# Kernel tuning notes

Hardware: AMD Instinct MI355X
Metric: run time of the kernel (lower is better)

Reference implementation:

```python
import jax, jax.numpy as jnp
import numpy as np

B, N, D_IN, D_HID, N_ITER = 32, 512, 256, 128, 10


def setup_inputs() -> dict:
    key = jax.random.key(0)
    ks = jax.random.split(key, 8)
    s = 1.0 / np.sqrt(D_IN)  # torch Linear default init range
    return {
        "Xh": jax.random.normal(ks[0], (B, N, D_IN), jnp.float32),
        "Xm": jax.random.normal(ks[1], (B, N, D_IN), jnp.float32),
        # position 0 is the root; tokens 1..len are valid
        "lengths": jax.random.randint(ks[2], (B,), N // 2, N),
        "Wh": jax.random.uniform(ks[3], (D_HID, D_IN), jnp.float32, -s, s),
        "bh": jax.random.uniform(ks[4], (D_HID,), jnp.float32, -s, s),
        "Wm": jax.random.uniform(ks[5], (D_HID, D_IN), jnp.float32, -s, s),
        "bm": jax.random.uniform(ks[6], (D_HID,), jnp.float32, -s, s),
        "V": 0.01 * jax.random.normal(ks[7], (D_HID, D_HID), jnp.float32),
    }


def _logZ(scores, lengths):
    """Matrix-tree log-partition for single-root nonprojective trees.

    scores: [B,N,N] arc scores, scores[b,h,m] = head h -> modifier m, index 0 = root.
    lengths: [B] number of real tokens (valid modifiers at 1..len).
    """
    Bn, Nn, _ = scores.shape
    idx = jnp.arange(Nn)
    tok = (idx[None, :] >= 1) & (idx[None, :] <= lengths[:, None])   # [B,N] valid modifiers
    head = idx[None, :] <= lengths[:, None]                          # [B,N] valid heads (incl. root)
    pair = head[:, :, None] & tok[:, None, :] & (idx[:, None] != idx[None, :])
    # stability shift: every tree has exactly `len` edges, so logZ shifts by len*c
    c = jax.lax.stop_gradient(
        jnp.max(jnp.where(pair, scores, -jnp.inf), axis=(1, 2)))
    A = jnp.where(pair, jnp.exp(scores - c[:, None, None]), 0.0)     # [B,N,N]
    r = A[:, 0, 1:]                                                  # root -> token weights [B,N-1]
    At = A[:, 1:, 1:]                                                # token -> token weights
    ar = jnp.arange(Nn - 1)
    # Laplacian L = diag(colsum) - At (diag of At is zero by pair mask)
    Lap = (-At).at[:, ar, ar].set(r + At.sum(axis=1))
    # Koo et al. (2007): replace first row with root weights
    Lhat = Lap.at[:, 0, :].set(r)
    # padded positions: identity rows to keep det unchanged
    Lhat = Lhat.at[:, ar, ar].add(jnp.where(tok[:, 1:], 0.0, 1.0))
    _, logabs = jnp.linalg.slogdet(Lhat)
    return logabs + lengths.astype(scores.dtype) * c


def _marginals(scores, lengths):
    """nonprojective_marginals: (logZ, entropy, mu) via grad of logZ."""
    def f(s):
        lz = _logZ(s, lengths)
        return lz.sum(), lz
    (_, logZ), Y = jax.value_and_grad(f, has_aux=True)(scores)
    entr = logZ - jnp.sum(Y * scores, axis=(1, 2))
    return logZ, entr, Y


def reference(Xh, Xm, lengths, Wh, bh, Wm, bm, V):
    # dropout=0 -> H_mask/M_mask are ones
    H0 = Xh @ Wh.T + bh          # h_mlp(Xh), invariant across iterations
    M0 = Xm @ Wm.T + bm          # m_mlp(Xm)
    H = jax.nn.relu(H0)
    M = jax.nn.relu(M0)
    scores = jnp.einsum("bhu,uv,bmv->bhm", H, V, M)
    logZ, entr, Y = _marginals(scores, lengths)
    for _ in range(1, N_ITER):
        Hn = jax.nn.relu(H0 + Y @ M @ V.T)                       # _update_H
        Mn = jax.nn.relu(M0 + jnp.swapaxes(Y, -2, -1) @ H @ V)   # _update_M
        scores = jnp.einsum("bhu,uv,bmv->bhm", Hn, V, Mn)
        logZ, entr, Y = _marginals(scores, lengths)
        H, M = Hn, Mn
    return scores, logZ, Y, entr
```

## Files before the change

kernel.cpp:

```cpp
#include <hip/hip_runtime.h>
#include <math.h>

constexpr int BB = 32;
constexpr int NN_ = 512;
constexpr int DIN = 256;
constexpr int DH = 128;
constexpr int NITER = 10;
constexpr long HSTR = (long)NN_ * DH;
constexpr long SSTR = (long)NN_ * NN_;
constexpr long LSTR = 512L * 512L;

__device__ __forceinline__ unsigned f2mono(float f) {
    unsigned u = __float_as_uint(f);
    return (u & 0x80000000u) ? ~u : (u | 0x80000000u);
}
__device__ __forceinline__ float mono2f(unsigned u) {
    return __uint_as_float((u & 0x80000000u) ? (u & 0x7fffffffu) : ~u);
}

__device__ __forceinline__ float invert128(float r[8][8], int tid,
        float (*RowP)[8][132], float (*ColPT)[8][132], float (*Rnew)[8][132])
{
    int tx = tid & 15, ty = tid >> 4;
    int lane = tid & 63, w = tid >> 6;
    int li = lane >> 3, lj = lane & 7;
    float lacc = 0.f;
    __syncthreads();
    for (int s8 = 0; s8 < 16; ++s8) {
        int p = s8 & 1;
        if (ty == s8) {
            #pragma unroll
            for (int i = 0; i < 8; ++i)
                #pragma unroll
                for (int j = 0; j < 8; ++j)
                    RowP[p][i][tx * 8 + j] = r[i][j];
        }
        if (tx == s8) {
            float sub = (ty == s8) ? 1.f : 0.f;
            #pragma unroll
            for (int i = 0; i < 8; ++i)
                #pragma unroll
                for (int j = 0; j < 8; ++j)
                    ColPT[p][j][ty * 8 + i] = r[i][j] - ((i == j) ? sub : 0.f);
        }
        __syncthreads();
        float d = RowP[p][li][s8 * 8 + lj];
        float prod = 1.f;
        #pragma unroll
        for (int s = 0; s < 8; ++s) {
            float pv = __shfl(d, s * 9);
            prod *= pv;
            float pinv = 1.0f / pv;
            float rv = __shfl(d, s * 8 + lj);
            float cv = __shfl(d, li * 8 + s);
            float nd;
            if (li == s && lj == s)  nd = pinv;
            else if (li == s)        nd = rv * pinv;
            else if (lj == s)        nd = -cv * pinv;
            else                     nd = d - cv * pinv * rv;
            d = nd;
        }
        lacc += logf(fabsf(prod));
        {
            int sr = li;
            int jq = w * 32 + lj * 4;
            float dsr[8];
            #pragma unroll
            for (int t = 0; t < 8; ++t) dsr[t] = __shfl(d, (lane & 56) + t);
            float a0 = 0.f, a1 = 0.f, a2 = 0.f, a3 = 0.f;
            #pragma unroll
            for (int t = 0; t < 8; ++t) {
                float4 rp = *(const float4*)&RowP[p][t][jq];
                a0 += dsr[t] * rp.x; a1 += dsr[t] * rp.y;
                a2 += dsr[t] * rp.z; a3 += dsr[t] * rp.w;
            }
            if ((jq >> 3) == s8) {
                if ((jq & 7) == 0) {
                    a0 = dsr[0] + ((sr == 0) ? 1.f : 0.f);
                    a1 = dsr[1] + ((sr == 1) ? 1.f : 0.f);
                    a2 = dsr[2] + ((sr == 2) ? 1.f : 0.f);
                    a3 = dsr[3] + ((sr == 3) ? 1.f : 0.f);
                } else {
                    a0 = dsr[4] + ((sr == 4) ? 1.f : 0.f);
                    a1 = dsr[5] + ((sr == 5) ? 1.f : 0.f);
                    a2 = dsr[6] + ((sr == 6) ? 1.f : 0.f);
                    a3 = dsr[7] + ((sr == 7) ? 1.f : 0.f);
                }
            }
            *(float4*)&Rnew[p][sr][jq] = make_float4(a0, a1, a2, a3);
        }
        __syncthreads();
        #pragma unroll
        for (int t = 0; t < 8; ++t) {
            float cp[8], rn[8];
            *(float4*)&cp[0] = *(const float4*)&ColPT[p][t][ty * 8];
            *(float4*)&cp[4] = *(const float4*)&ColPT[p][t][ty * 8 + 4];
            *(float4*)&rn[0] = *(const float4*)&Rnew[p][t][tx * 8];
            *(float4*)&rn[4] = *(const float4*)&Rnew[p][t][tx * 8 + 4];
            #pragma unroll
            for (int i = 0; i < 8; ++i)
                #pragma unroll
                for (int j = 0; j < 8; ++j)
                    r[i][j] -= cp[i] * rn[j];
        }
    }
    return lacc;
}

template<int AMODE, int BMODE, int EPI>
__global__ __launch_bounds__(256) void gemm64(
    const float* __restrict__ A, const float* __restrict__ Bm,
    float* __restrict__ C, const float* __restrict__ Dp, float* __restrict__ C2,
    int Mdim, int Ndim, int Kdim,
    long sA, long sB, long sC, long sD)
{
    constexpr int BK = 16;
    __shared__ float As[BK][64 + 4];
    __shared__ float Bs[BK][64 + 4];
    int b = blockIdx.z;
    const float* Ab = A + (long)b * sA;
    const float* Bb = Bm + (long)b * sB;
    int m0 = blockIdx.x * 64, n0 = blockIdx.y * 64;
    int tid = threadIdx.x;
    int tx = tid & 15, ty = tid >> 4;
    float acc[4][4] = {};

    int arow, acol, brow, bcol;
    if (AMODE == 0) { arow = tid >> 2; acol = (tid & 3) * 4; }
    else            { arow = tid >> 4; acol = (tid & 15) * 4; }
    if (BMODE == 0) { brow = tid >> 4; bcol = (tid & 15) * 4; }
    else            { brow = tid >> 2; bcol = (tid & 3) * 4; }

    float4 av, bv;
    if (AMODE == 0) av = *(const float4*)(Ab + (long)(m0 + arow) * Kdim + acol);
    else            av = *(const float4*)(Ab + (long)(0 + arow) * Mdim + m0 + acol);
    if (BMODE == 0) bv = *(const float4*)(Bb + (long)(0 + brow) * Ndim + n0 + bcol);
    else            bv = *(const float4*)(Bb + (long)(n0 + brow) * Kdim + bcol);

    for (int k0 = 0; k0 < Kdim; k0 += BK) {
        __syncthreads();
        if (AMODE == 0) {
            As[acol + 0][arow] = av.x; As[acol + 1][arow] = av.y;
            As[acol + 2][arow] = av.z; As[acol + 3][arow] = av.w;
        } else {
            *(float4*)&As[arow][acol] = av;
        }
        if (BMODE == 0) {
            *(float4*)&Bs[brow][bcol] = bv;
        } else {
            Bs[bcol + 0][brow] = bv.x; Bs[bcol + 1][brow] = bv.y;
            Bs[bcol + 2][brow] = bv.z; Bs[bcol + 3][brow] = bv.w;
        }
        float4 av2, bv2;
        if (k0 + BK < Kdim) {
            int k1 = k0 + BK;
            if (AMODE == 0) av2 = *(const float4*)(Ab + (long)(m0 + arow) * Kdim + k1 + acol);
            else            av2 = *(const float4*)(Ab + (long)(k1 + arow) * Mdim + m0 + acol);
            if (BMODE == 0) bv2 = *(const float4*)(Bb + (long)(k1 + brow) * Ndim + n0 + bcol);
            else            bv2 = *(const float4*)(Bb + (long)(n0 + brow) * Kdim + k1 + bcol);
        }
        __syncthreads();
        #pragma unroll
        for (int k = 0; k < BK; ++k) {
            float4 a4 = *(const float4*)&As[k][ty * 4];
            float4 b4 = *(const float4*)&Bs[k][tx * 4];
            float avv[4] = {a4.x, a4.y, a4.z, a4.w};
            float bvv[4] = {b4.x, b4.y, b4.z, b4.w};
            #pragma unroll
            for (int i = 0; i < 4; ++i)
                #pragma unroll
                for (int j = 0; j < 4; ++j)
                    acc[i][j] += avv[i] * bvv[j];
        }
        av = av2; bv = bv2;
    }

    int r0 = m0 + ty * 4, c0 = n0 + tx * 4;
    if (EPI == 0) {
        float* Cb = C + (long)b * sC;
        #pragma unroll
        for (int i = 0; i < 4; ++i)
            *(float4*)(Cb + (long)(r0 + i) * Ndim + c0) =
                make_float4(acc[i][0], acc[i][1], acc[i][2], acc[i][3]);
    } else if (EPI == 1) {
        float4 bias = *(const float4*)(Dp + c0);
        float bb4[4] = {bias.x, bias.y, bias.z, bias.w};
        #pragma unroll
        for (int i = 0; i < 4; ++i) {
            float pre[4];
            #pragma unroll
            for (int j = 0; j < 4; ++j) pre[j] = acc[i][j] + bb4[j];
            *(float4*)(C2 + (long)(r0 + i) * Ndim + c0) =
                make_float4(pre[0], pre[1], pre[2], pre[3]);
            *(float4*)(C + (long)(r0 + i) * Ndim + c0) =
                make_float4(fmaxf(pre[0], 0.f), fmaxf(pre[1], 0.f),
                            fmaxf(pre[2], 0.f), fmaxf(pre[3], 0.f));
        }
    } else {
        const float* Db = Dp + (long)b * sD;
        float* Cb = C + (long)b * sC;
        #pragma unroll
        for (int i = 0; i < 4; ++i) {
            float4 d = *(const float4*)(Db + (long)(r0 + i) * Ndim + c0);
            float pre[4] = {acc[i][0] + d.x, acc[i][1] + d.y,
                            acc[i][2] + d.z, acc[i][3] + d.w};
            *(float4*)(Cb + (long)(r0 + i) * Ndim + c0) =
                make_float4(fmaxf(pre[0], 0.f), fmaxf(pre[1], 0.f),
                            fmaxf(pre[2], 0.f), fmaxf(pre[3], 0.f));
        }
    }
}

__global__ __launch_bounds__(256) void score_gemm(
    const float* __restrict__ A, const float* __restrict__ Bm,
    float* __restrict__ C, const int* __restrict__ len,
    unsigned* __restrict__ cu)
{
    int b = blockIdx.z;
    const float* Ab = A + (long)b * HSTR;
    const float* Bb = Bm + (long)b * HSTR;
    int m0 = blockIdx.x * 128, n0 = blockIdx.y * 128;
    int tid = threadIdx.x, tx = tid & 15, ty = tid >> 4;
    __shared__ float As[8][132];
    __shared__ float Bs[8][132];
    float acc[8][8] = {};
    int row = tid >> 1, kq = (tid & 1) << 2;
    float4 av = *(const float4*)(Ab + (long)(m0 + row) * DH + kq);
    float4 bv = *(const float4*)(Bb + (long)(n0 + row) * DH + kq);
    for (int kc = 0; kc < DH; kc += 8) {
        __syncthreads();
        As[kq + 0][row] = av.x; As[kq + 1][row] = av.y;
        As[kq + 2][row] = av.z; As[kq + 3][row] = av.w;
        Bs[kq + 0][row] = bv.x; Bs[kq + 1][row] = bv.y;
        Bs[kq + 2][row] = bv.z; Bs[kq + 3][row] = bv.w;
        float4 av2, bv2;
        if (kc + 8 < DH) {
            av2 = *(const float4*)(Ab + (long)(m0 + row) * DH + kc + 8 + kq);
            bv2 = *(const float4*)(Bb + (long)(n0 + row) * DH + kc + 8 + kq);
        }
        __syncthreads();
        #pragma unroll
        for (int k = 0; k < 8; ++k) {
            float a[8], bb[8];
            *(float4*)&a[0] = *(float4*)&As[k][ty * 8];
            *(float4*)&a[4] = *(float4*)&As[k][ty * 8 + 4];
            *(float4*)&bb[0] = *(float4*)&Bs[k][tx * 8];
            *(float4*)&bb[4] = *(float4*)&Bs[k][tx * 8 + 4];
            #pragma unroll
            for (int i = 0; i < 8; ++i)
                #pragma unroll
                for (int j = 0; j < 8; ++j) acc[i][j] += a[i] * bb[j];
        }
        av = av2; bv = bv2;
    }
    int L = len[b];
    float vmax = -3.0e38f;
    float* Cb = C + (long)b * SSTR;
    #pragma unroll
    for (int i = 0; i < 8; ++i) {
        int h = m0 + ty * 8 + i;
        bool hok = (h <= L);
        *(float4*)(Cb + (long)h * NN_ + n0 + tx * 8) =
            make_float4(acc[i][0], acc[i][1], acc[i][2], acc[i][3]);
        *(float4*)(Cb + (long)h * NN_ + n0 + tx * 8 + 4) =
            make_float4(acc[i][4], acc[i][5], acc[i][6], acc[i][7]);
        #pragma unroll
        for (int j = 0; j < 8; ++j) {
            int m = n0 + tx * 8 + j;
            if (hok && m >= 1 && m <= L && m != h) vmax = fmaxf(vmax, acc[i][j]);
        }
    }
    __syncthreads();
    float* red = &As[0][0];
    red[tid] = vmax; __syncthreads();
    for (int off = 128; off; off >>= 1) {
        if (tid < off) red[tid] = fmaxf(red[tid], red[tid + off]);
        __syncthreads();
    }
    if (tid == 0) atomicMax(&cu[b], f2mono(red[0]));
}

__global__ void zero_scal(float* scal) {
    if (threadIdx.x < 96) scal[threadIdx.x] = 0.f;
}

__global__ __launch_bounds__(256) void colsum_k(const float* __restrict__ sc,
                                                const int* __restrict__ len,
                                                const unsigned* __restrict__ cu,
                                                float* __restrict__ colsum)
{
    int b = blockIdx.x, yb = blockIdx.y;
    int tid = threadIdx.x, lane = tid & 63, w = tid >> 6;
    int L = len[b];
    float c = mono2f(cu[b]);
    int m = yb * 64 + lane;
    const float* S = sc + (long)b * SSTR;
    float s = 0.f;
    bool mv = (m >= 1 && m <= L);
    if (mv) {
        for (int h = 1 + w; h < NN_; h += 4) {
            if (h <= L && h != m) s += expf(S[(long)h * NN_ + m] - c);
        }
    }
    __shared__ float part[4][64];
    part[w][lane] = s; __syncthreads();
    if (tid < 64)
        colsum[(long)b * NN_ + yb * 64 + tid] =
            part[0][tid] + part[1][tid] + part[2][tid] + part[3][tid];
}

__global__ __launch_bounds__(256) void build_rows(const float* __restrict__ sc,
                                                  const int* __restrict__ len,
                                                  const unsigned* __restrict__ cu,
                                                  const float* __restrict__ colsum,
                                                  float* __restrict__ Lm,
                                                  float* __restrict__ Fb0,
                                                  float* __restrict__ logdet)
{
    __shared__ float sm[6][8][132];
    int b = blockIdx.x;
    int tid = threadIdx.x;
    int L = len[b];
    float c = mono2f(cu[b]);
    const float* S = sc + (long)b * SSTR;
    const float* cs = colsum + (long)b * NN_;

    if (blockIdx.y == 0) {
        int tx = tid & 15, ty = tid >> 4;
        float r[8][8];
        #pragma unroll
        for (int i = 0; i < 8; ++i) {
            int gi = ty * 8 + i;
            #pragma unroll
            for (int j = 0; j < 8; ++j) {
                int gj = tx * 8 + j;
                int tm = gj + 1;
                bool mv = (tm <= L);
                float v;
                if (gi == 0) {
                    v = mv ? expf(S[tm] - c) : 0.f;
                } else if (gi == gj) {
                    float rv = mv ? expf(S[tm] - c) : 0.f;
                    v = rv + cs[tm] + (mv ? 0.f : 1.f);
                } else {
                    int h = gi + 1;
                    v = (h <= L && mv) ? -expf(S[(long)h * NN_ + tm] - c) : 0.f;
                }
                r[i][j] = v;
            }
        }
        float lacc = invert128(r, tid,
                               (float(*)[8][132])&sm[0],
                               (float(*)[8][132])&sm[2],
                               (float(*)[8][132])&sm[4]);
        float* Ab = Lm + (long)b * LSTR;
        #pragma unroll
        for (int i = 0; i < 8; ++i) {
            *(float4*)(Ab + (long)(ty * 8 + i) * 512 + tx * 8) =
                make_float4(r[i][0], r[i][1], r[i][2], r[i][3]);
            *(float4*)(Ab + (long)(ty * 8 + i) * 512 + tx * 8 + 4) =
                make_float4(r[i][4], r[i][5], r[i][6], r[i][7]);
        }
        if (tid == 0) atomicAdd(&logdet[b], lacc);
        return;
    }

    int i0 = (blockIdx.y - 1) * 8;
    #pragma unroll
    for (int r = 0; r < 8; ++r) {
        int i = i0 + r;
        float* Lrow = Lm + (long)b * LSTR + (long)i * 512;
        float* Frow = Fb0 + (long)b * HSTR + (long)i * 128;
        #pragma unroll
        for (int q = 0; q < 2; ++q) {
            int j = tid + q * 256;
            float v;
            if (i == 511 || j == 511) {
                v = (i == j) ? 1.f : 0.f;
            } else {
                int tm = j + 1;
                bool mv = (tm <= L);
                if (i == 0) {
                    v = mv ? expf(S[tm] - c) : 0.f;
                } else if (i == j) {
                    float rv = mv ? expf(S[tm] - c) : 0.f;
                    v = rv + cs[tm] + ((tm > L) ? 1.f : 0.f);
                } else {
                    int h = i + 1;
                    v = (h <= L && mv) ? -expf(S[(long)h * NN_ + tm] - c) : 0.f;
                }
            }
            if (!(i < 128 && j < 128)) Lrow[j] = v;
            if (q == 0 && j < 128 && i >= 128) Frow[j] = v;
        }
    }
}

__global__ __launch_bounds__(256) void gj_panel(float* __restrict__ Lm,
                                                float* __restrict__ Fnext, int kb)
{
    int b = blockIdx.x, j = blockIdx.y;
    int jt = j + (j >= kb);
    int tid = threadIdx.x;
    float* base = Lm + (long)b * LSTR;
    const float* D = base + (long)(kb * 128) * 512 + kb * 128;
    float* Aj = base + (long)(kb * 128) * 512 + jt * 128;
    __shared__ float Ds_[8][132];
    __shared__ float Asj[8][132];
    int tx = tid & 15, ty = tid >> 4;
    int drow = tid >> 1, dkq = (tid & 1) << 2;
    int akr = tid >> 5, acq = (tid & 31) << 2;
    float acc[8][8] = {};
    float4 dv = *(const float4*)(D + (long)drow * 512 + dkq);
    float4 ajv = *(const float4*)(Aj + (long)akr * 512 + acq);
    for (int kc = 0; kc < 128; kc += 8) {
        __syncthreads();
        Ds_[dkq + 0][drow] = dv.x; Ds_[dkq + 1][drow] = dv.y;
        Ds_[dkq + 2][drow] = dv.z; Ds_[dkq + 3][drow] = dv.w;
        *(float4*)&Asj[akr][acq] = ajv;
        float4 dv2, ajv2;
        if (kc + 8 < 128) {
            dv2 = *(const float4*)(D + (long)drow * 512 + kc + 8 + dkq);
            ajv2 = *(const float4*)(Aj + (long)(kc + 8 + akr) * 512 + acq);
        }
        __syncthreads();
        #pragma unroll
        for (int k = 0; k < 8; ++k) {
            float a[8], bv[8];
            *(float4*)&a[0] = *(float4*)&Ds_[k][ty * 8];
            *(float4*)&a[4] = *(float4*)&Ds_[k][ty * 8 + 4];
            *(float4*)&bv[0] = *(float4*)&Asj[k][tx * 8];
            *(float4*)&bv[4] = *(float4*)&Asj[k][tx * 8 + 4];
            #pragma unroll
            for (int i = 0; i < 8; ++i)
                #pragma unroll
                for (int jj = 0; jj < 8; ++jj) acc[i][jj] += a[i] * bv[jj];
        }
        dv = dv2; ajv = ajv2;
    }
    bool dual = (jt == kb + 1);
    float* Fn = Fnext + (long)b * HSTR + (long)(kb * 128) * 128;
    #pragma unroll
    for (int i = 0; i < 8; ++i) {
        float4 o0 = make_float4(acc[i][0], acc[i][1], acc[i][2], acc[i][3]);
        float4 o1 = make_float4(acc[i][4], acc[i][5], acc[i][6], acc[i][7]);
        *(float4*)(Aj + (long)(ty * 8 + i) * 512 + tx * 8) = o0;
        *(float4*)(Aj + (long)(ty * 8 + i) * 512 + tx * 8 + 4) = o1;
        if (dual) {
            *(float4*)(Fn + (long)(ty * 8 + i) * 128 + tx * 8) = o0;
            *(float4*)(Fn + (long)(ty * 8 + i) * 128 + tx * 8 + 4) = o1;
        }
    }
}

template<int FUSE>
__global__ __launch_bounds__(256) void gj_update(float* __restrict__ Lm,
                                                 const float* __restrict__ Fbuf,
                                                 float* __restrict__ Fnext,
                                                 float* __restrict__ logdet, int kb)
{
    __shared__ float sm[FUSE ? 6 : 2][8][132];
    int b = blockIdx.x;
    int it = blockIdx.y;
    int jt = blockIdx.z;
    int ib = it + (it >= kb);
    int tid = threadIdx.x, tx = tid & 15, ty = tid >> 4;
    float* base = Lm + (long)b * LSTR;
    const float* F = Fbuf + (long)b * HSTR + (long)(ib * 128) * 128;
    const float* R = base + (long)(kb * 128) * 512 + jt * 128;
    float* Cb = base + (long)(ib * 128) * 512 + jt * 128;
    float (*Fs)[132] = sm[0];
    float (*Rs)[132] = sm[1];
    int frow = tid >> 1, fkq = (tid & 1) << 2;
    int rkr = tid >> 5, rcq = (tid & 31) << 2;
    float acc[8][8] = {};
    float4 fv = *(const float4*)(F + (long)frow * 128 + fkq);
    float4 rv = *(const float4*)(R + (long)rkr * 512 + rcq);
    for (int kc = 0; kc < 128; kc += 8) {
        __syncthreads();
        Fs[fkq + 0][frow] = fv.x; Fs[fkq + 1][frow] = fv.y;
        Fs[fkq + 2][frow] = fv.z; Fs[fkq + 3][frow] = fv.w;
        *(float4*)&Rs[rkr][rcq] = rv;
        float4 fv2, rv2;
        if (kc + 8 < 128) {
            fv2 = *(const float4*)(F + (long)frow * 128 + kc + 8 + fkq);
            rv2 = *(const float4*)(R + (long)(kc + 8 + rkr) * 512 + rcq);
        }
        __syncthreads();
        #pragma unroll
        for (int k = 0; k < 8; ++k) {
            float a[8], bv[8];
            *(float4*)&a[0] = *(float4*)&Fs[k][ty * 8];
            *(float4*)&a[4] = *(float4*)&Fs[k][ty * 8 + 4];
            *(float4*)&bv[0] = *(float4*)&Rs[k][tx * 8];
            *(float4*)&bv[4] = *(float4*)&Rs[k][tx * 8 + 4];
            #pragma unroll
            for (int i = 0; i < 8; ++i)
                #pragma unroll
                for (int j = 0; j < 8; ++j) acc[i][j] += a[i] * bv[j];
        }
        fv = fv2; rv = rv2;
    }
    if (FUSE && ib == kb + 1 && jt == kb + 1) {
        #pragma unroll
        for (int i = 0; i < 8; ++i) {
            float4 o0 = *(const float4*)(Cb + (long)(ty * 8 + i) * 512 + tx * 8);
            float4 o1 = *(const float4*)(Cb + (long)(ty * 8 + i) * 512 + tx * 8 + 4);
            acc[i][0] = o0.x - acc[i][0]; acc[i][1] = o0.y - acc[i][1];
            acc[i][2] = o0.z - acc[i][2]; acc[i][3] = o0.w - acc[i][3];
            acc[i][4] = o1.x - acc[i][4]; acc[i][5] = o1.y - acc[i][5];
            acc[i][6] = o1.z - acc[i][6]; acc[i][7] = o1.w - acc[i][7];
        }
        float lacc = invert128(acc, tid,
                               (float(*)[8][132])&sm[0],
                               (float(*)[8][132])&sm[FUSE ? 2 : 0],
                               (float(*)[8][132])&sm[FUSE ? 4 : 0]);
        #pragma unroll
        for (int i = 0; i < 8; ++i) {
            *(float4*)(Cb + (long)(ty * 8 + i) * 512 + tx * 8) =
                make_float4(acc[i][0], acc[i][1], acc[i][2], acc[i][3]);
            *(float4*)(Cb + (long)(ty * 8 + i) * 512 + tx * 8 + 4) =
                make_float4(acc[i][4], acc[i][5], acc[i][6], acc[i][7]);
        }
        if (tid == 0) atomicAdd(&logdet[b], lacc);
        return;
    }
    bool dual = (jt == kb + 1);
    float* Fn = Fnext + (long)b * HSTR + (long)(ib * 128) * 128;
    if (jt == kb) {
        #pragma unroll
        for (int i = 0; i < 8; ++i) {
            *(float4*)(Cb + (long)(ty * 8 + i) * 512 + tx * 8) =
                make_float4(-acc[i][0], -acc[i][1], -acc[i][2], -acc[i][3]);
            *(float4*)(Cb + (long)(ty * 8 + i) * 512 + tx * 8 + 4) =
                make_float4(-acc[i][4], -acc[i][5], -acc[i][6], -acc[i][7]);
        }
    } else {
        #pragma unroll
        for (int i = 0; i < 8; ++i) {
            float4 o0 = *(const float4*)(Cb + (long)(ty * 8 + i) * 512 + tx * 8);
            float4 o1 = *(const float4*)(Cb + (long)(ty * 8 + i) * 512 + tx * 8 + 4);
            o0 = make_float4(o0.x - acc[i][0], o0.y - acc[i][1],
                             o0.z - acc[i][2], o0.w - acc[i][3]);
            o1 = make_float4(o1.x - acc[i][4], o1.y - acc[i][5],
                             o1.z - acc[i][6], o1.w - acc[i][7]);
            *(float4*)(Cb + (long)(ty * 8 + i) * 512 + tx * 8) = o0;
            *(float4*)(Cb + (long)(ty * 8 + i) * 512 + tx * 8 + 4) = o1;
            if (dual) {
                *(float4*)(Fn + (long)(ty * 8 + i) * 128 + tx * 8) = o0;
                *(float4*)(Fn + (long)(ty * 8 + i) * 128 + tx * 8 + 4) = o1;
            }
        }
    }
}

__global__ __launch_bounds__(256) void y_k(const float* __restrict__ sc,
                                           const float* __restrict__ Binv,
                                           const int* __restrict__ len,
                                           const unsigned* __restrict__ cu,
                                           float* __restrict__ Y,
                                           float* __restrict__ Ssum)
{
    int b = blockIdx.x;
    int ht = blockIdx.y >> 3, mt = blockIdx.y & 7;
    int h0 = ht * 64, m0 = mt * 64;
    int tid = threadIdx.x;
    int L = len[b];
    float c = mono2f(cu[b]);
    const float* S = sc + (long)b * SSTR;
    const float* Bi = Binv + (long)b * LSTR;
    float* Yb = Y + (long)b * SSTR;
    __shared__ float Bs[64][65];
    __shared__ float Ds[64], C0s[64];
    {
        int hh = tid & 63, m4 = tid >> 6;
        int col = h0 + hh - 1;
        for (int mm = m4; mm < 64; mm += 4) {
            int row = m0 + mm - 1;
            Bs[mm][hh] = (row >= 0 && col >= 0) ? Bi[(long)row * 512 + col] : 0.f;
        }
    }
    if (tid < 64) {
        int row = m0 + tid - 1;
        Ds[tid] = (row >= 0) ? Bi[(long)row * 512 + row] : 0.f;
    } else if (tid < 128) {
        int mm = tid - 64, row = m0 + mm - 1;
        C0s[mm] = (row >= 0) ? Bi[(long)row * 512] : 0.f;
    }
    __syncthreads();
    int mm = tid & 63, hq = tid >> 6;
    int m = m0 + mm;
    float lsum = 0.f;
    bool mvalid = (m >= 1 && m <= L);
    float dterm = (m >= 2) ? Ds[mm] : 0.f;
    #pragma unroll
    for (int hi = 0; hi < 16; ++hi) {
        int hh = hq * 16 + hi;
        int h = h0 + hh;
        float s = S[(long)h * NN_ + m];
        float y = 0.f;
        if (mvalid && h <= L && h != m) {
            float a = expf(s - c);
            float g;
            if (h == 0) g = C0s[mm] + dterm;
            else g = dterm - ((h >= 2) ? Bs[mm][hh] : 0.f);
            y = a * g;
        }
        Yb[(long)h * NN_ + m] = y;
        lsum += y * s;
    }
    __shared__ float red[256];
    red[tid] = lsum; __syncthreads();
    for (int off = 128; off; off >>= 1) {
        if (tid < off) red[tid] += red[tid + off];
        __syncthreads();
    }
    if (tid == 0) atomicAdd(&Ssum[b], red[0]);
}

__global__ void fin_k(const int* __restrict__ len, unsigned* __restrict__ cu,
                      float* __restrict__ logdet, float* __restrict__ Ssum,
                      float* __restrict__ outLogZ, float* __restrict__ outEntr)
{
    int b = threadIdx.x;
    if (b < 32) {
        float c = mono2f(cu[b]);
        float lz = logdet[b] + (float)len[b] * c;
        outLogZ[b] = lz;
        outEntr[b] = lz - Ssum[b];
        cu[b] = 0u;
        logdet[b] = 0.f;
        Ssum[b] = 0.f;
    }
}

extern "C" void kernel_launch(void* const* d_in, const int* in_sizes, int n_in,
                              void* d_out, int out_size, void* d_ws, size_t ws_size,
                              hipStream_t stream)
{
    const float* Xh = (const float*)d_in[0];
    const float* Xm = (const float*)d_in[1];
    const int*   len = (const int*)d_in[2];
    const float* Wh = (const float*)d_in[3];
    const float* bh = (const float*)d_in[4];
    const float* Wm = (const float*)d_in[5];
    const float* bm = (const float*)d_in[6];
    const float* V  = (const float*)d_in[7];

    float* ws = (float*)d_ws;
    constexpr long U = 2097152;
    float* H0 = ws;
    float* M0 = ws + U;
    float* Ha = ws + 2 * U;
    float* Ma = ws + 3 * U;
    float* Hb = ws + 4 * U;
    float* Mb = ws + 5 * U;
    float* T1 = ws + 6 * U;
    float* Yt = ws + 7 * U;
    float* Lm = ws + 8 * U;
    float* cs = ws + 12 * U;
    float* scal = ws + 12 * U + 16384;
    unsigned* cu = (unsigned*)scal;
    float* logdet = scal + 32;
    float* Ssum = scal + 64;

    float* Sout = (float*)d_out;
    float* outLogZ = (float*)d_out + 8388608;
    float* Yout = (float*)d_out + 8388640;
    float* outEntr = (float*)d_out + 8388640 + 8388608;

    zero_scal<<<1, 96, 0, stream>>>(scal);

    gemm64<0,1,1><<<dim3(256, 2, 1), 256, 0, stream>>>(
        Xh, Wh, Ha, bh, H0, 16384, DH, DIN, 0, 0, 0, 0);
    gemm64<0,1,1><<<dim3(256, 2, 1), 256, 0, stream>>>(
        Xm, Wm, Ma, bm, M0, 16384, DH, DIN, 0, 0, 0, 0);

    float* Hc = Ha; float* Mc = Ma; float* Hn = Hb; float* Mn = Mb;
    for (int t = 0; t < NITER; ++t) {
        if (t > 0) {
            gemm64<0,1,0><<<dim3(8,2,BB),256,0,stream>>>(
                Mc, V, Yt, nullptr, nullptr, 512, DH, DH, HSTR, 0, HSTR, 0);
            gemm64<0,0,2><<<dim3(8,2,BB),256,0,stream>>>(
                Yout, Yt, Hn, H0, nullptr, 512, DH, 512, SSTR, HSTR, HSTR, HSTR);
            gemm64<1,0,2><<<dim3(8,2,BB),256,0,stream>>>(
                Yout, T1, Mn, M0, nullptr, 512, DH, 512, SSTR, HSTR, HSTR, HSTR);
            { float* tmp = Hc; Hc = Hn; Hn = tmp; }
            { float* tmp = Mc; Mc = Mn; Mn = tmp; }
        }
        gemm64<0,0,0><<<dim3(8,2,BB),256,0,stream>>>(
            Hc, V, T1, nullptr, nullptr, 512, DH, DH, HSTR, 0, HSTR, 0);
        score_gemm<<<dim3(4,4,BB),256,0,stream>>>(T1, Mc, Sout, len, cu);

        colsum_k<<<dim3(BB,8),256,0,stream>>>(Sout, len, cu, cs);
        build_rows<<<dim3(BB,65),256,0,stream>>>(Sout, len, cu, cs, Lm, Yt, logdet);

        float* Fbufs[2] = {Yt, Hn};
        for (int kb = 0; kb < 4; ++kb) {
            float* Fcur  = Fbufs[kb & 1];
            float* Fnext = Fbufs[(kb + 1) & 1];
            gj_panel<<<dim3(BB,3),256,0,stream>>>(Lm, Fnext, kb);
            if (kb < 3)
                gj_update<1><<<dim3(BB,3,4),256,0,stream>>>(Lm, Fcur, Fnext, logdet, kb);
            else
                gj_update<0><<<dim3(BB,3,4),256,0,stream>>>(Lm, Fcur, Fnext, logdet, kb);
        }
        y_k<<<dim3(BB,64),256,0,stream>>>(Sout, Lm, len, cu, Yout, Ssum);
        fin_k<<<1,32,0,stream>>>(len, cu, logdet, Ssum, outLogZ, outEntr);
    }
}
```

Measured before the change: 5.692 ms.

## Move diagonal block inversion into panel kernel and widen GJ kernels to 512 threads

The 128x128 diagonal-block inversion moves out of the tail of gj_update, where a single block ran it serially, and into the start of the panel kernel. Every panel block now redundantly inverts the pivot block held in registers, and only block 0 writes it back and adds to logdet. Both the panel and update GEMMs switch to 512 threads with 8x4 per-thread tiles and a K-step of 16, aiming for more parallelism and shorter serial tails. The cost is that the inversion is computed three times per batch, and invert128 runs with half the threads idle.

```diff
diff --git a/kernel.cpp b/kernel.cpp
--- a/kernel.cpp
+++ b/kernel.cpp
@@ -24,18 +24,19 @@
     int tx = tid & 15, ty = tid >> 4;
     int lane = tid & 63, w = tid >> 6;
     int li = lane >> 3, lj = lane & 7;
+    const bool act = (tid < 256);
     float lacc = 0.f;
     __syncthreads();
     for (int s8 = 0; s8 < 16; ++s8) {
         int p = s8 & 1;
-        if (ty == s8) {
+        if (act && ty == s8) {
             #pragma unroll
             for (int i = 0; i < 8; ++i)
                 #pragma unroll
                 for (int j = 0; j < 8; ++j)
                     RowP[p][i][tx * 8 + j] = r[i][j];
         }
-        if (tx == s8) {
+        if (act && tx == s8) {
             float sub = (ty == s8) ? 1.f : 0.f;
             #pragma unroll
             for (int i = 0; i < 8; ++i)
@@ -61,7 +62,7 @@
             d = nd;
         }
         lacc += logf(fabsf(prod));
-        {
+        if (act) {
             int sr = li;
             int jq = w * 32 + lj * 4;
             float dsr[8];
@@ -90,18 +91,20 @@
             *(float4*)&Rnew[p][sr][jq] = make_float4(a0, a1, a2, a3);
         }
         __syncthreads();
-        #pragma unroll
-        for (int t = 0; t < 8; ++t) {
-            float cp[8], rn[8];
-            *(float4*)&cp[0] = *(const float4*)&ColPT[p][t][ty * 8];
-            *(float4*)&cp[4] = *(const float4*)&ColPT[p][t][ty * 8 + 4];
-            *(float4*)&rn[0] = *(const float4*)&Rnew[p][t][tx * 8];
-            *(float4*)&rn[4] = *(const float4*)&Rnew[p][t][tx * 8 + 4];
-            #pragma unroll
-            for (int i = 0; i < 8; ++i)
-                #pragma unroll
-                for (int j = 0; j < 8; ++j)
-                    r[i][j] -= cp[i] * rn[j];
+        if (act) {
+            #pragma unroll
+            for (int t = 0; t < 8; ++t) {
+                float cp[8], rn[8];
+                *(float4*)&cp[0] = *(const float4*)&ColPT[p][t][ty * 8];
+                *(float4*)&cp[4] = *(const float4*)&ColPT[p][t][ty * 8 + 4];
+                *(float4*)&rn[0] = *(const float4*)&Rnew[p][t][tx * 8];
+                *(float4*)&rn[4] = *(const float4*)&Rnew[p][t][tx * 8 + 4];
+                #pragma unroll
+                for (int i = 0; i < 8; ++i)
+                    #pragma unroll
+                    for (int j = 0; j < 8; ++j)
+                        r[i][j] -= cp[i] * rn[j];
+            }
         }
     }
     return lacc;
@@ -396,160 +399,161 @@
     }
 }
 
-__global__ __launch_bounds__(256) void gj_panel(float* __restrict__ Lm,
-                                                float* __restrict__ Fnext, int kb)
-{
+__global__ __launch_bounds__(512) void gj_panel_inv(
+    float* __restrict__ Lm, const float* __restrict__ Fcur,
+    float* __restrict__ Fnext, float* __restrict__ logdet, int kb)
+{
+    __shared__ float sm[6 * 8 * 132];
+    float (*Ds)[132]  = (float (*)[132])sm;
+    float (*Asj)[132] = (float (*)[132])(sm + 16 * 132);
     int b = blockIdx.x, j = blockIdx.y;
     int jt = j + (j >= kb);
     int tid = threadIdx.x;
+    int tx = tid & 15, ty = tid >> 4;
     float* base = Lm + (long)b * LSTR;
-    const float* D = base + (long)(kb * 128) * 512 + kb * 128;
+    float r[8][8] = {};
+    if (kb == 0) {
+        if (tid < 256) {
+            const float* D0 = base;
+            #pragma unroll
+            for (int i = 0; i < 8; ++i) {
+                *(float4*)&r[i][0] = *(const float4*)(D0 + (long)(ty * 8 + i) * 512 + tx * 8);
+                *(float4*)&r[i][4] = *(const float4*)(D0 + (long)(ty * 8 + i) * 512 + tx * 8 + 4);
+            }
+        }
+    } else {
+        if (tid < 256) {
+            const float* T = Fcur + (long)b * HSTR + (long)(kb * 128) * 128;
+            #pragma unroll
+            for (int i = 0; i < 8; ++i) {
+                *(float4*)&r[i][0] = *(const float4*)(T + (long)(ty * 8 + i) * 128 + tx * 8);
+                *(float4*)&r[i][4] = *(const float4*)(T + (long)(ty * 8 + i) * 128 + tx * 8 + 4);
+            }
+        }
+        float lacc = invert128(r, tid,
+                               (float (*)[8][132])sm,
+                               (float (*)[8][132])(sm + 2 * 8 * 132),
+                               (float (*)[8][132])(sm + 4 * 8 * 132));
+        if (j == 0) {
+            if (tid < 256) {
+                float* Dd = base + (long)(kb * 128) * 512 + kb * 128;
+                #pragma unroll
+                for (int i = 0; i < 8; ++i) {
+                    *(float4*)(Dd + (long)(ty * 8 + i) * 512 + tx * 8) =
+                        make_float4(r[i][0], r[i][1], r[i][2], r[i][3]);
+                    *(float4*)(Dd + (long)(ty * 8 + i) * 512 + tx * 8 + 4) =
+                        make_float4(r[i][4], r[i][5], r[i][6], r[i][7]);
+                }
+            }
+            if (tid == 0) atomicAdd(&logdet[b], lacc);
+        }
+    }
+
+    int tx2 = tid & 31, ty2 = tid >> 5;
     float* Aj = base + (long)(kb * 128) * 512 + jt * 128;
-    __shared__ float Ds_[8][132];
-    __shared__ float Asj[8][132];
-    int tx = tid & 15, ty = tid >> 4;
-    int drow = tid >> 1, dkq = (tid & 1) << 2;
     int akr = tid >> 5, acq = (tid & 31) << 2;
-    float acc[8][8] = {};
-    float4 dv = *(const float4*)(D + (long)drow * 512 + dkq);
+    float acc[8][4] = {};
     float4 ajv = *(const float4*)(Aj + (long)akr * 512 + acq);
-    for (int kc = 0; kc < 128; kc += 8) {
-        __syncthreads();
-        Ds_[dkq + 0][drow] = dv.x; Ds_[dkq + 1][drow] = dv.y;
-        Ds_[dkq + 2][drow] = dv.z; Ds_[dkq + 3][drow] = dv.w;
+    for (int kc = 0; kc < 128; kc += 16) {
+        __syncthreads();
+        if (tid < 256 && (tx >> 1) == (kc >> 4)) {
+            int kloc = (tx & 1) * 8;
+            #pragma unroll
+            for (int i = 0; i < 8; ++i)
+                #pragma unroll
+                for (int jj = 0; jj < 8; ++jj)
+                    Ds[kloc + jj][ty * 8 + i] = r[i][jj];
+        }
         *(float4*)&Asj[akr][acq] = ajv;
-        float4 dv2, ajv2;
-        if (kc + 8 < 128) {
-            dv2 = *(const float4*)(D + (long)drow * 512 + kc + 8 + dkq);
-            ajv2 = *(const float4*)(Aj + (long)(kc + 8 + akr) * 512 + acq);
-        }
-        __syncthreads();
-        #pragma unroll
-        for (int k = 0; k < 8; ++k) {
-            float a[8], bv[8];
-            *(float4*)&a[0] = *(float4*)&Ds_[k][ty * 8];
-            *(float4*)&a[4] = *(float4*)&Ds_[k][ty * 8 + 4];
-            *(float4*)&bv[0] = *(float4*)&Asj[k][tx * 8];
-            *(float4*)&bv[4] = *(float4*)&Asj[k][tx * 8 + 4];
+        float4 ajv2;
+        if (kc + 16 < 128)
+            ajv2 = *(const float4*)(Aj + (long)(kc + 16 + akr) * 512 + acq);
+        __syncthreads();
+        #pragma unroll
+        for (int k = 0; k < 16; ++k) {
+            float a[8], bv[4];
+            *(float4*)&a[0] = *(const float4*)&Ds[k][ty2 * 8];
+            *(float4*)&a[4] = *(const float4*)&Ds[k][ty2 * 8 + 4];
+            *(float4*)&bv[0] = *(const float4*)&Asj[k][tx2 * 4];
             #pragma unroll
             for (int i = 0; i < 8; ++i)
                 #pragma unroll
-                for (int jj = 0; jj < 8; ++jj) acc[i][jj] += a[i] * bv[jj];
-        }
-        dv = dv2; ajv = ajv2;
+                for (int jj = 0; jj < 4; ++jj)
+                    acc[i][jj] += a[i] * bv[jj];
+        }
+        ajv = ajv2;
     }
     bool dual = (jt == kb + 1);
     float* Fn = Fnext + (long)b * HSTR + (long)(kb * 128) * 128;
     #pragma unroll
     for (int i = 0; i < 8; ++i) {
-        float4 o0 = make_float4(acc[i][0], acc[i][1], acc[i][2], acc[i][3]);
-        float4 o1 = make_float4(acc[i][4], acc[i][5], acc[i][6], acc[i][7]);
-        *(float4*)(Aj + (long)(ty * 8 + i) * 512 + tx * 8) = o0;
-        *(float4*)(Aj + (long)(ty * 8 + i) * 512 + tx * 8 + 4) = o1;
-        if (dual) {
-            *(float4*)(Fn + (long)(ty * 8 + i) * 128 + tx * 8) = o0;
-            *(float4*)(Fn + (long)(ty * 8 + i) * 128 + tx * 8 + 4) = o1;
-        }
-    }
-}
-
-template<int FUSE>
-__global__ __launch_bounds__(256) void gj_update(float* __restrict__ Lm,
-                                                 const float* __restrict__ Fbuf,
-                                                 float* __restrict__ Fnext,
-                                                 float* __restrict__ logdet, int kb)
-{
-    __shared__ float sm[FUSE ? 6 : 2][8][132];
+        float4 o = make_float4(acc[i][0], acc[i][1], acc[i][2], acc[i][3]);
+        *(float4*)(Aj + (long)(ty2 * 8 + i) * 512 + tx2 * 4) = o;
+        if (dual) *(float4*)(Fn + (long)(ty2 * 8 + i) * 128 + tx2 * 4) = o;
+    }
+}
+
+__global__ __launch_bounds__(512, 4) void gj_update(
+    float* __restrict__ Lm, const float* __restrict__ Fbuf,
+    float* __restrict__ Fnext, int kb)
+{
+    __shared__ float Fs[16][132];
+    __shared__ float Rs[16][132];
     int b = blockIdx.x;
     int it = blockIdx.y;
     int jt = blockIdx.z;
     int ib = it + (it >= kb);
-    int tid = threadIdx.x, tx = tid & 15, ty = tid >> 4;
+    int tid = threadIdx.x;
+    int tx = tid & 31, ty = tid >> 5;
     float* base = Lm + (long)b * LSTR;
     const float* F = Fbuf + (long)b * HSTR + (long)(ib * 128) * 128;
     const float* R = base + (long)(kb * 128) * 512 + jt * 128;
     float* Cb = base + (long)(ib * 128) * 512 + jt * 128;
-    float (*Fs)[132] = sm[0];
-    float (*Rs)[132] = sm[1];
-    int frow = tid >> 1, fkq = (tid & 1) << 2;
+    int frow = tid >> 2, fkq = (tid & 3) << 2;
     int rkr = tid >> 5, rcq = (tid & 31) << 2;
-    float acc[8][8] = {};
+    float acc[8][4] = {};
     float4 fv = *(const float4*)(F + (long)frow * 128 + fkq);
     float4 rv = *(const float4*)(R + (long)rkr * 512 + rcq);
-    for (int kc = 0; kc < 128; kc += 8) {
+    for (int kc = 0; kc < 128; kc += 16) {
         __syncthreads();
         Fs[fkq + 0][frow] = fv.x; Fs[fkq + 1][frow] = fv.y;
         Fs[fkq + 2][frow] = fv.z; Fs[fkq + 3][frow] = fv.w;
         *(float4*)&Rs[rkr][rcq] = rv;
         float4 fv2, rv2;
-        if (kc + 8 < 128) {
-            fv2 = *(const float4*)(F + (long)frow * 128 + kc + 8 + fkq);
-            rv2 = *(const float4*)(R + (long)(kc + 8 + rkr) * 512 + rcq);
-        }
-        __syncthreads();
-        #pragma unroll
-        for (int k = 0; k < 8; ++k) {
-            float a[8], bv[8];
-            *(float4*)&a[0] = *(float4*)&Fs[k][ty * 8];
-            *(float4*)&a[4] = *(float4*)&Fs[k][ty * 8 + 4];
-            *(float4*)&bv[0] = *(float4*)&Rs[k][tx * 8];
-            *(float4*)&bv[4] = *(float4*)&Rs[k][tx * 8 + 4];
+        if (kc + 16 < 128) {
+            fv2 = *(const float4*)(F + (long)frow * 128 + kc + 16 + fkq);
+            rv2 = *(const float4*)(R + (long)(kc + 16 + rkr) * 512 + rcq);
+        }
+        __syncthreads();
+        #pragma unroll
+        for (int k = 0; k < 16; ++k) {
+            float a[8], bv[4];
+            *(float4*)&a[0] = *(const float4*)&Fs[k][ty * 8];
+            *(float4*)&a[4] = *(const float4*)&Fs[k][ty * 8 + 4];
+            *(float4*)&bv[0] = *(const float4*)&Rs[k][tx * 4];
             #pragma unroll
             for (int i = 0; i < 8; ++i)
                 #pragma unroll
-                for (int j = 0; j < 8; ++j) acc[i][j] += a[i] * bv[j];
+                for (int jj = 0; jj < 4; ++jj)
+                    acc[i][jj] += a[i] * bv[jj];
         }
         fv = fv2; rv = rv2;
-    }
-    if (FUSE && ib == kb + 1 && jt == kb + 1) {
-        #pragma unroll
-        for (int i = 0; i < 8; ++i) {
-            float4 o0 = *(const float4*)(Cb + (long)(ty * 8 + i) * 512 + tx * 8);
-            float4 o1 = *(const float4*)(Cb + (long)(ty * 8 + i) * 512 + tx * 8 + 4);
-            acc[i][0] = o0.x - acc[i][0]; acc[i][1] = o0.y - acc[i][1];
-            acc[i][2] = o0.z - acc[i][2]; acc[i][3] = o0.w - acc[i][3];
-            acc[i][4] = o1.x - acc[i][4]; acc[i][5] = o1.y - acc[i][5];
-            acc[i][6] = o1.z - acc[i][6]; acc[i][7] = o1.w - acc[i][7];
-        }
-        float lacc = invert128(acc, tid,
-                               (float(*)[8][132])&sm[0],
-                               (float(*)[8][132])&sm[FUSE ? 2 : 0],
-                               (float(*)[8][132])&sm[FUSE ? 4 : 0]);
-        #pragma unroll
-        for (int i = 0; i < 8; ++i) {
-            *(float4*)(Cb + (long)(ty * 8 + i) * 512 + tx * 8) =
-                make_float4(acc[i][0], acc[i][1], acc[i][2], acc[i][3]);
-            *(float4*)(Cb + (long)(ty * 8 + i) * 512 + tx * 8 + 4) =
-                make_float4(acc[i][4], acc[i][5], acc[i][6], acc[i][7]);
-        }
-        if (tid == 0) atomicAdd(&logdet[b], lacc);
-        return;
     }
     bool dual = (jt == kb + 1);
     float* Fn = Fnext + (long)b * HSTR + (long)(ib * 128) * 128;
     if (jt == kb) {
         #pragma unroll
+        for (int i = 0; i < 8; ++i)
+            *(float4*)(Cb + (long)(ty * 8 + i) * 512 + tx * 4) =
+                make_float4(-acc[i][0], -acc[i][1], -acc[i][2], -acc[i][3]);
+    } else {
+        #pragma unroll
         for (int i = 0; i < 8; ++i) {
-            *(float4*)(Cb + (long)(ty * 8 + i) * 512 + tx * 8) =
-                make_float4(-acc[i][0], -acc[i][1], -acc[i][2], -acc[i][3]);
-            *(float4*)(Cb + (long)(ty * 8 + i) * 512 + tx * 8 + 4) =
-                make_float4(-acc[i][4], -acc[i][5], -acc[i][6], -acc[i][7]);
-        }
-    } else {
-        #pragma unroll
-        for (int i = 0; i < 8; ++i) {
-            float4 o0 = *(const float4*)(Cb + (long)(ty * 8 + i) * 512 + tx * 8);
-            float4 o1 = *(const float4*)(Cb + (long)(ty * 8 + i) * 512 + tx * 8 + 4);
-            o0 = make_float4(o0.x - acc[i][0], o0.y - acc[i][1],
-                             o0.z - acc[i][2], o0.w - acc[i][3]);
-            o1 = make_float4(o1.x - acc[i][4], o1.y - acc[i][5],
-                             o1.z - acc[i][6], o1.w - acc[i][7]);
-            *(float4*)(Cb + (long)(ty * 8 + i) * 512 + tx * 8) = o0;
-            *(float4*)(Cb + (long)(ty * 8 + i) * 512 + tx * 8 + 4) = o1;
-            if (dual) {
-                *(float4*)(Fn + (long)(ty * 8 + i) * 128 + tx * 8) = o0;
-                *(float4*)(Fn + (long)(ty * 8 + i) * 128 + tx * 8 + 4) = o1;
-            }
+            float4 o = *(const float4*)(Cb + (long)(ty * 8 + i) * 512 + tx * 4);
+            o = make_float4(o.x - acc[i][0], o.y - acc[i][1],
+                            o.z - acc[i][2], o.w - acc[i][3]);
+            *(float4*)(Cb + (long)(ty * 8 + i) * 512 + tx * 4) = o;
+            if (dual) *(float4*)(Fn + (long)(ty * 8 + i) * 128 + tx * 4) = o;
         }
     }
 }
@@ -699,11 +703,8 @@
         for (int kb = 0; kb < 4; ++kb) {
             float* Fcur  = Fbufs[kb & 1];
             float* Fnext = Fbufs[(kb + 1) & 1];
-            gj_panel<<<dim3(BB,3),256,0,stream>>>(Lm, Fnext, kb);
-            if (kb < 3)
-                gj_update<1><<<dim3(BB,3,4),256,0,stream>>>(Lm, Fcur, Fnext, logdet, kb);
-            else
-                gj_update<0><<<dim3(BB,3,4),256,0,stream>>>(Lm, Fcur, Fnext, logdet, kb);
+            gj_panel_inv<<<dim3(BB,3),512,0,stream>>>(Lm, Fcur, Fnext, logdet, kb);
+            gj_update<<<dim3(BB,3,4),512,0,stream>>>(Lm, Fcur, Fnext, kb);
         }
         y_k<<<dim3(BB,64),256,0,stream>>>(Sout, Lm, len, cu, Yout, Ssum);
         fin_k<<<1,32,0,stream>>>(len, cu, logdet, Ssum, outLogZ, outEntr);
```

Result: slower. 6.917 ms (+21.5%).

## Split Gauss-Jordan update into 64x64 tiles and separate diagonal-block inversion kernel

Applied to the files above, without the earlier changes.

The blocked Gauss-Jordan trailing update now uses 64x64 output tiles with a 4x4 per-thread micro-tile, launched as 4x more blocks, so each batch has more parallel work and the device fills better. The fused inversion of the next diagonal block, previously done inside one update block, moves into its own inv_k kernel launched after the update. This adds a kernel launch per panel step and lowers per-thread register reuse, in exchange for shorter, better-balanced update blocks. invert128 gains an active-thread guard that is always true at 256 threads.

```diff
diff --git a/kernel.cpp b/kernel.cpp
--- a/kernel.cpp
+++ b/kernel.cpp
@@ -24,18 +24,19 @@
     int tx = tid & 15, ty = tid >> 4;
     int lane = tid & 63, w = tid >> 6;
     int li = lane >> 3, lj = lane & 7;
+    const bool act = (tid < 256);
     float lacc = 0.f;
     __syncthreads();
     for (int s8 = 0; s8 < 16; ++s8) {
         int p = s8 & 1;
-        if (ty == s8) {
+        if (act && ty == s8) {
             #pragma unroll
             for (int i = 0; i < 8; ++i)
                 #pragma unroll
                 for (int j = 0; j < 8; ++j)
                     RowP[p][i][tx * 8 + j] = r[i][j];
         }
-        if (tx == s8) {
+        if (act && tx == s8) {
             float sub = (ty == s8) ? 1.f : 0.f;
             #pragma unroll
             for (int i = 0; i < 8; ++i)
@@ -61,7 +62,7 @@
             d = nd;
         }
         lacc += logf(fabsf(prod));
-        {
+        if (act) {
             int sr = li;
             int jq = w * 32 + lj * 4;
             float dsr[8];
@@ -90,18 +91,20 @@
             *(float4*)&Rnew[p][sr][jq] = make_float4(a0, a1, a2, a3);
         }
         __syncthreads();
-        #pragma unroll
-        for (int t = 0; t < 8; ++t) {
-            float cp[8], rn[8];
-            *(float4*)&cp[0] = *(const float4*)&ColPT[p][t][ty * 8];
-            *(float4*)&cp[4] = *(const float4*)&ColPT[p][t][ty * 8 + 4];
-            *(float4*)&rn[0] = *(const float4*)&Rnew[p][t][tx * 8];
-            *(float4*)&rn[4] = *(const float4*)&Rnew[p][t][tx * 8 + 4];
-            #pragma unroll
-            for (int i = 0; i < 8; ++i)
+        if (act) {
+            #pragma unroll
+            for (int t = 0; t < 8; ++t) {
+                float cp[8], rn[8];
+                *(float4*)&cp[0] = *(const float4*)&ColPT[p][t][ty * 8];
+                *(float4*)&cp[4] = *(const float4*)&ColPT[p][t][ty * 8 + 4];
+                *(float4*)&rn[0] = *(const float4*)&Rnew[p][t][tx * 8];
+                *(float4*)&rn[4] = *(const float4*)&Rnew[p][t][tx * 8 + 4];
                 #pragma unroll
-                for (int j = 0; j < 8; ++j)
-                    r[i][j] -= cp[i] * rn[j];
+                for (int i = 0; i < 8; ++i)
+                    #pragma unroll
+                    for (int j = 0; j < 8; ++j)
+                        r[i][j] -= cp[i] * rn[j];
+            }
         }
     }
     return lacc;
@@ -453,105 +456,101 @@
     }
 }
 
-template<int FUSE>
-__global__ __launch_bounds__(256) void gj_update(float* __restrict__ Lm,
-                                                 const float* __restrict__ Fbuf,
-                                                 float* __restrict__ Fnext,
-                                                 float* __restrict__ logdet, int kb)
-{
-    __shared__ float sm[FUSE ? 6 : 2][8][132];
+__global__ __launch_bounds__(256) void gj_update64(
+    float* __restrict__ Lm, const float* __restrict__ Fbuf,
+    float* __restrict__ Fnext, int kb)
+{
+    constexpr int BK = 16;
+    __shared__ float Fs[BK][68];
+    __shared__ float Rs[BK][68];
     int b = blockIdx.x;
     int it = blockIdx.y;
-    int jt = blockIdx.z;
     int ib = it + (it >= kb);
-    int tid = threadIdx.x, tx = tid & 15, ty = tid >> 4;
+    int sub = blockIdx.z;
+    int jt = sub >> 2;
+    int quad = sub & 3;
+    int r0 = (quad >> 1) * 64, c0 = (quad & 1) * 64;
+    int tid = threadIdx.x;
+    int tx = tid & 15, ty = tid >> 4;
     float* base = Lm + (long)b * LSTR;
-    const float* F = Fbuf + (long)b * HSTR + (long)(ib * 128) * 128;
-    const float* R = base + (long)(kb * 128) * 512 + jt * 128;
-    float* Cb = base + (long)(ib * 128) * 512 + jt * 128;
-    float (*Fs)[132] = sm[0];
-    float (*Rs)[132] = sm[1];
-    int frow = tid >> 1, fkq = (tid & 1) << 2;
-    int rkr = tid >> 5, rcq = (tid & 31) << 2;
-    float acc[8][8] = {};
+    const float* F = Fbuf + (long)b * HSTR + (long)(ib * 128 + r0) * 128;
+    const float* R = base + (long)(kb * 128) * 512 + jt * 128 + c0;
+    float* Cb = base + (long)(ib * 128 + r0) * 512 + jt * 128 + c0;
+    int frow = tid >> 2, fkq = (tid & 3) << 2;
+    int rkr = tid >> 4, rcq = (tid & 15) << 2;
+    float acc[4][4] = {};
     float4 fv = *(const float4*)(F + (long)frow * 128 + fkq);
     float4 rv = *(const float4*)(R + (long)rkr * 512 + rcq);
-    for (int kc = 0; kc < 128; kc += 8) {
+    for (int kc = 0; kc < 128; kc += BK) {
         __syncthreads();
         Fs[fkq + 0][frow] = fv.x; Fs[fkq + 1][frow] = fv.y;
         Fs[fkq + 2][frow] = fv.z; Fs[fkq + 3][frow] = fv.w;
         *(float4*)&Rs[rkr][rcq] = rv;
         float4 fv2, rv2;
-        if (kc + 8 < 128) {
-            fv2 = *(const float4*)(F + (long)frow * 128 + kc + 8 + fkq);
-            rv2 = *(const float4*)(R + (long)(kc + 8 + rkr) * 512 + rcq);
-        }
-        __syncthreads();
-        #pragma unroll
-        for (int k = 0; k < 8; ++k) {
-            float a[8], bv[8];
-            *(float4*)&a[0] = *(float4*)&Fs[k][ty * 8];
-            *(float4*)&a[4] = *(float4*)&Fs[k][ty * 8 + 4];
-            *(float4*)&bv[0] = *(float4*)&Rs[k][tx * 8];
-            *(float4*)&bv[4] = *(float4*)&Rs[k][tx * 8 + 4];
-            #pragma unroll
-            for (int i = 0; i < 8; ++i)
+        if (kc + BK < 128) {
+            fv2 = *(const float4*)(F + (long)frow * 128 + kc + BK + fkq);
+            rv2 = *(const float4*)(R + (long)(kc + BK + rkr) * 512 + rcq);
+        }
+        __syncthreads();
+        #pragma unroll
+        for (int k = 0; k < BK; ++k) {
+            float4 a4 = *(const float4*)&Fs[k][ty * 4];
+            float4 b4 = *(const float4*)&Rs[k][tx * 4];
+            float a[4] = {a4.x, a4.y, a4.z, a4.w};
+            float bb[4] = {b4.x, b4.y, b4.z, b4.w};
+            #pragma unroll
+            for (int i = 0; i < 4; ++i)
                 #pragma unroll
-                for (int j = 0; j < 8; ++j) acc[i][j] += a[i] * bv[j];
+                for (int j = 0; j < 4; ++j)
+                    acc[i][j] += a[i] * bb[j];
         }
         fv = fv2; rv = rv2;
     }
-    if (FUSE && ib == kb + 1 && jt == kb + 1) {
-        #pragma unroll
-        for (int i = 0; i < 8; ++i) {
-            float4 o0 = *(const float4*)(Cb + (long)(ty * 8 + i) * 512 + tx * 8);
-            float4 o1 = *(const float4*)(Cb + (long)(ty * 8 + i) * 512 + tx * 8 + 4);
-            acc[i][0] = o0.x - acc[i][0]; acc[i][1] = o0.y - acc[i][1];
-            acc[i][2] = o0.z - acc[i][2]; acc[i][3] = o0.w - acc[i][3];
-            acc[i][4] = o1.x - acc[i][4]; acc[i][5] = o1.y - acc[i][5];
-            acc[i][6] = o1.z - acc[i][6]; acc[i][7] = o1.w - acc[i][7];
-        }
-        float lacc = invert128(acc, tid,
-                               (float(*)[8][132])&sm[0],
-                               (float(*)[8][132])&sm[FUSE ? 2 : 0],
-                               (float(*)[8][132])&sm[FUSE ? 4 : 0]);
-        #pragma unroll
-        for (int i = 0; i < 8; ++i) {
-            *(float4*)(Cb + (long)(ty * 8 + i) * 512 + tx * 8) =
-                make_float4(acc[i][0], acc[i][1], acc[i][2], acc[i][3]);
-            *(float4*)(Cb + (long)(ty * 8 + i) * 512 + tx * 8 + 4) =
-                make_float4(acc[i][4], acc[i][5], acc[i][6], acc[i][7]);
-        }
-        if (tid == 0) atomicAdd(&logdet[b], lacc);
-        return;
-    }
     bool dual = (jt == kb + 1);
-    float* Fn = Fnext + (long)b * HSTR + (long)(ib * 128) * 128;
+    float* Fn = Fnext + (long)b * HSTR + (long)(ib * 128 + r0) * 128 + c0;
     if (jt == kb) {
         #pragma unroll
-        for (int i = 0; i < 8; ++i) {
-            *(float4*)(Cb + (long)(ty * 8 + i) * 512 + tx * 8) =
+        for (int i = 0; i < 4; ++i)
+            *(float4*)(Cb + (long)(ty * 4 + i) * 512 + tx * 4) =
                 make_float4(-acc[i][0], -acc[i][1], -acc[i][2], -acc[i][3]);
-            *(float4*)(Cb + (long)(ty * 8 + i) * 512 + tx * 8 + 4) =
-                make_float4(-acc[i][4], -acc[i][5], -acc[i][6], -acc[i][7]);
-        }
     } else {
         #pragma unroll
-        for (int i = 0; i < 8; ++i) {
-            float4 o0 = *(const float4*)(Cb + (long)(ty * 8 + i) * 512 + tx * 8);
-            float4 o1 = *(const float4*)(Cb + (long)(ty * 8 + i) * 512 + tx * 8 + 4);
-            o0 = make_float4(o0.x - acc[i][0], o0.y - acc[i][1],
-                             o0.z - acc[i][2], o0.w - acc[i][3]);
-            o1 = make_float4(o1.x - acc[i][4], o1.y - acc[i][5],
-                             o1.z - acc[i][6], o1.w - acc[i][7]);
-            *(float4*)(Cb + (long)(ty * 8 + i) * 512 + tx * 8) = o0;
-            *(float4*)(Cb + (long)(ty * 8 + i) * 512 + tx * 8 + 4) = o1;
-            if (dual) {
-                *(float4*)(Fn + (long)(ty * 8 + i) * 128 + tx * 8) = o0;
-                *(float4*)(Fn + (long)(ty * 8 + i) * 128 + tx * 8 + 4) = o1;
-            }
-        }
-    }
+        for (int i = 0; i < 4; ++i) {
+            float4 o = *(const float4*)(Cb + (long)(ty * 4 + i) * 512 + tx * 4);
+            o = make_float4(o.x - acc[i][0], o.y - acc[i][1],
+                            o.z - acc[i][2], o.w - acc[i][3]);
+            *(float4*)(Cb + (long)(ty * 4 + i) * 512 + tx * 4) = o;
+            if (dual) *(float4*)(Fn + (long)(ty * 4 + i) * 128 + tx * 4) = o;
+        }
+    }
+}
+
+__global__ __launch_bounds__(256) void inv_k(float* __restrict__ Lm,
+                                             float* __restrict__ logdet, int kb)
+{
+    __shared__ float sm[6][8][132];
+    int b = blockIdx.x;
+    int tid = threadIdx.x;
+    int tx = tid & 15, ty = tid >> 4;
+    float* Dd = Lm + (long)b * LSTR + (long)(kb * 128) * 512 + kb * 128;
+    float r[8][8];
+    #pragma unroll
+    for (int i = 0; i < 8; ++i) {
+        *(float4*)&r[i][0] = *(const float4*)(Dd + (long)(ty * 8 + i) * 512 + tx * 8);
+        *(float4*)&r[i][4] = *(const float4*)(Dd + (long)(ty * 8 + i) * 512 + tx * 8 + 4);
+    }
+    float lacc = invert128(r, tid,
+                           (float(*)[8][132])&sm[0],
+                           (float(*)[8][132])&sm[2],
+                           (float(*)[8][132])&sm[4]);
+    #pragma unroll
+    for (int i = 0; i < 8; ++i) {
+        *(float4*)(Dd + (long)(ty * 8 + i) * 512 + tx * 8) =
+            make_float4(r[i][0], r[i][1], r[i][2], r[i][3]);
+        *(float4*)(Dd + (long)(ty * 8 + i) * 512 + tx * 8 + 4) =
+            make_float4(r[i][4], r[i][5], r[i][6], r[i][7]);
+    }
+    if (tid == 0) atomicAdd(&logdet[b], lacc);
 }
 
 __global__ __launch_bounds__(256) void y_k(const float* __restrict__ sc,
@@ -700,10 +699,9 @@
             float* Fcur  = Fbufs[kb & 1];
             float* Fnext = Fbufs[(kb + 1) & 1];
             gj_panel<<<dim3(BB,3),256,0,stream>>>(Lm, Fnext, kb);
+            gj_update64<<<dim3(BB,3,16),256,0,stream>>>(Lm, Fcur, Fnext, kb);
             if (kb < 3)
-                gj_update<1><<<dim3(BB,3,4),256,0,stream>>>(Lm, Fcur, Fnext, logdet, kb);
-            else
-                gj_update<0><<<dim3(BB,3,4),256,0,stream>>>(Lm, Fcur, Fnext, logdet, kb);
+                inv_k<<<dim3(BB),256,0,stream>>>(Lm, logdet, kb + 1);
         }
         y_k<<<dim3(BB,64),256,0,stream>>>(Sout, Lm, len, cu, Yout, Ssum);
         fin_k<<<1,32,0,stream>>>(len, cu, logdet, Ssum, outLogZ, outEntr);
```

After: 5.793 ms. About the same (+1.8%).
